# Kernel optimization log

Measured on AMD Instinct MI355X. Metric: run time of the kernel, lower is better.

## Reference

```python
import jax, jax.numpy as jnp
import numpy as np

N, ID, OD, M, S, L = 65536, 16, 8, 1024, 8, 64


def setup_inputs() -> dict:
    key = jax.random.key(0)
    k1, k2, k3, k4, k5, k6 = jax.random.split(key, 6)
    return {
        "x": jax.random.normal(k1, (N, ID), dtype=jnp.float32),
        "inducing_locations": jax.random.uniform(k2, (M, ID), dtype=jnp.float32),
        "inducing_weights": jax.random.normal(k3, (S, OD, M), dtype=jnp.float32),
        "prior_frequency": jax.random.normal(k4, (OD, ID, L), dtype=jnp.float32),
        "prior_phase": jax.random.uniform(k5, (OD, L), dtype=jnp.float32, maxval=2 * np.pi),
        "prior_weights": jax.random.normal(k6, (S, OD, L), dtype=jnp.float32),
    }


def _rbf_matrix(x, z):
    # ExponentiatedQuadratic with amplitude=1, length_scale=1:
    # k(x,z) = exp(-0.5 * ||x - z||^2)
    x2 = jnp.sum(x * x, axis=-1)[:, None]          # [N,1]
    z2 = jnp.sum(z * z, axis=-1)[None, :]          # [1,M]
    sq = jnp.maximum(x2 + z2 - 2.0 * (x @ z.T), 0.0)
    return jnp.exp(-0.5 * sq)                      # [N,M]


def reference(x, inducing_locations, inducing_weights, prior_frequency, prior_phase, prior_weights):
    # ---- prior (random Fourier features) ----
    # spectral_weights for unit RBF: outer_weights = ones((OD,L)), inner_weights = ones((ID,))
    # rescaled_x = x / 1 = x
    # basis_fn_inner_prod: [OD, N, L]
    inner = jnp.einsum('ni,oil->onl', x, prior_frequency)
    basis_fn = jnp.cos(inner + prior_phase[:, None, :])              # [OD,N,L]
    basis_weight = jnp.sqrt(2.0 / prior_frequency.shape[-1]) * prior_weights  # [S,OD,L]
    f_prior = jnp.einsum('onl,sol->son', basis_fn, basis_weight)     # [S,OD,N]

    # ---- data term (kernel matrix + matvec) ----
    K = _rbf_matrix(x, inducing_locations)                           # [N,M]
    f_data = jnp.einsum('nm,som->son', K, inducing_weights)          # [S,OD,N]

    return f_prior + f_data
```

## Files before the change

### kernel.cpp

```cpp
#include <hip/hip_runtime.h>
#include <hip/hip_bf16.h>

#define N_PTS 65536
#define LOG2E 1.4426950408889634f

typedef __attribute__((ext_vector_type(8))) short short8;
typedef __attribute__((ext_vector_type(4))) short short4v;
typedef __attribute__((ext_vector_type(4))) float float4v;

#if __has_builtin(__builtin_amdgcn_exp2f)
#define EXP2F(x) __builtin_amdgcn_exp2f(x)
#else
#define EXP2F(x) exp2f(x)
#endif

__device__ __forceinline__ short f2b(float f) {
    __hip_bfloat16 h = __float2bfloat16(f);
    return *(short*)&h;
}
__device__ __forceinline__ float b2f(short s) {
    __hip_bfloat16 h = *(__hip_bfloat16*)&s;
    return __bfloat162float(h);
}

__global__ __launch_bounds__(256) void prep_kernel(
    const float* __restrict__ z, const float* __restrict__ W,
    const float* __restrict__ F, const float* __restrict__ pw,
    short* __restrict__ zb, short* __restrict__ FbB,
    short* __restrict__ BWd, short* __restrict__ Wtb,
    float* __restrict__ z2h)
{
    int t = blockIdx.x * 256 + threadIdx.x;
    if (t < 16384) {
        zb[t] = f2b(LOG2E * z[t]);
    } else if (t < 17408) {
        int m = t - 16384;
        const float4v* zp = (const float4v*)(z + (size_t)m * 16);
        float s = 0.f;
        #pragma unroll
        for (int k = 0; k < 4; k++) {
            float4v v = zp[k];
            float a0 = b2f(f2b(v.x)), a1 = b2f(f2b(v.y));
            float a2 = b2f(f2b(v.z)), a3 = b2f(f2b(v.w));
            s += a0 * a0 + a1 * a1 + a2 * a2 + a3 * a3;
        }
        z2h[m] = 0.5f * LOG2E * s;
    } else if (t < 25600) {
        int p = t - 17408;
        int o = p >> 10, l = (p >> 4) & 63, i = p & 15;
        FbB[p] = f2b(F[o * 1024 + i * 64 + l]);
    } else if (t < 58368) {
        int p = t - 25600;
        int so = p >> 9, ol = p & 511, o = ol >> 6;
        float v = ((so & 7) == o) ? 0.17677669529663687f * pw[so * 64 + (ol & 63)] : 0.f;
        BWd[p] = f2b(v);
    } else if (t < 123904) {
        int p = t - 58368;
        Wtb[p] = f2b(W[p]);
    }
}

__global__ __launch_bounds__(256, 3) void fused_kernel(
    const float* __restrict__ x, const float* __restrict__ ph,
    const short* __restrict__ zb, const short* __restrict__ FbB,
    const short* __restrict__ BWd, const short* __restrict__ Wtb,
    const float* __restrict__ z2h, float* __restrict__ out)
{
    __shared__ __align__(16) char smem[34816];
    short* tiles = (short*)smem;
    float* phc   = (float*)(smem + 16384);
    float* nz2   = (float*)(smem + 18432);
    float* x2c   = (float*)(smem + 22528);
    float* rbufA = (float*)smem;
    float* rbufB = (float*)(smem + 17408);

    const int tid = threadIdx.x;
    const int lane = tid & 63, w = tid >> 6;
    const int q = lane >> 4, c = lane & 15;
    const int n0 = blockIdx.x * 64;

    for (int i = tid; i < 512; i += 256) phc[i] = ph[i];
    for (int i = tid; i < 1024; i += 256) nz2[i] = -z2h[i];
    if (tid < 64) {
        float s = 0.f;
        const float4v* xr = (const float4v*)(x + (size_t)(n0 + tid) * 16);
        #pragma unroll
        for (int k = 0; k < 4; k++) {
            float4v v = xr[k];
            float a0 = b2f(f2b(v.x)), a1 = b2f(f2b(v.y));
            float a2 = b2f(f2b(v.z)), a3 = b2f(f2b(v.w));
            s += a0 * a0 + a1 * a1 + a2 * a2 + a3 * a3;
        }
        x2c[tid] = 0.5f * LOG2E * s;
    }

    short8 ax[4];
    #pragma unroll
    for (int nt = 0; nt < 4; nt++) {
        ax[nt] = (short8)0;
        if (q < 2) {
            const float4v* xp = (const float4v*)(x + (size_t)(n0 + nt * 16 + c) * 16 + q * 8);
            float4v v0 = xp[0], v1 = xp[1];
            ax[nt][0] = f2b(v0.x); ax[nt][1] = f2b(v0.y);
            ax[nt][2] = f2b(v0.z); ax[nt][3] = f2b(v0.w);
            ax[nt][4] = f2b(v1.x); ax[nt][5] = f2b(v1.y);
            ax[nt][6] = f2b(v1.z); ax[nt][7] = f2b(v1.w);
        }
    }

    float4v acc[4][4];
    #pragma unroll
    for (int a = 0; a < 4; a++)
        #pragma unroll
        for (int nt = 0; nt < 4; nt++) acc[a][nt] = (float4v)(0.f);

    __syncthreads();

    char* myt = (char*)tiles + w * 4096;
    const int swz = (c & 3) << 4;
    const int wb0 = (c * 64 + q * 8) ^ swz;
    const int wb1 = (c * 64 + 32 + q * 8) ^ swz;
    const int rb0 = (c * 64 + q * 16) ^ swz;

    const int mbase = w * 256;
    #pragma unroll 2
    for (int mb = 0; mb < 8; mb++) {
        const int m0 = mbase + mb * 32;
        #pragma unroll
        for (int mh = 0; mh < 2; mh++) {
            short8 bz = (short8)0;
            if (q < 2) bz = *(const short8*)(zb + (size_t)(m0 + mh * 16 + c) * 16 + q * 8);
            float4v c0 = *(const float4v*)(nz2 + m0 + mh * 16 + 4 * q);
            const int wb = mh ? wb1 : wb0;
            #pragma unroll
            for (int nt = 0; nt < 4; nt++) {
                float4v d = __builtin_amdgcn_mfma_f32_16x16x32_bf16(bz, ax[nt], c0, 0, 0, 0);
                short4v pk;
                pk[0] = f2b(EXP2F(d[0])); pk[1] = f2b(EXP2F(d[1]));
                pk[2] = f2b(EXP2F(d[2])); pk[3] = f2b(EXP2F(d[3]));
                *(short4v*)(myt + nt * 1024 + wb) = pk;
            }
        }
        short8 aw[4];
        #pragma unroll
        for (int a = 0; a < 4; a++)
            aw[a] = *(const short8*)(Wtb + (size_t)(a * 16 + c) * 1024 + m0 + q * 8);
        #pragma unroll
        for (int nt = 0; nt < 4; nt++) {
            short8 bb = *(const short8*)(myt + nt * 1024 + rb0);
            #pragma unroll
            for (int a = 0; a < 4; a++)
                acc[a][nt] = __builtin_amdgcn_mfma_f32_16x16x32_bf16(aw[a], bb, acc[a][nt], 0, 0, 0);
        }
    }

    #pragma unroll
    for (int nt = 0; nt < 4; nt++) {
        float sxv = EXP2F(-x2c[nt * 16 + c]);
        #pragma unroll
        for (int a = 0; a < 4; a++) acc[a][nt] *= sxv;
    }

    const int lbase = w * 128;
    #pragma unroll 2
    for (int lb = 0; lb < 4; lb++) {
        const int l0 = lbase + lb * 32;
        #pragma unroll
        for (int mh = 0; mh < 2; mh++) {
            short8 bf = (short8)0;
            if (q < 2) bf = *(const short8*)(FbB + (size_t)(l0 + mh * 16 + c) * 16 + q * 8);
            float4v c0 = *(const float4v*)(phc + l0 + mh * 16 + 4 * q);
            const int wb = mh ? wb1 : wb0;
            #pragma unroll
            for (int nt = 0; nt < 4; nt++) {
                float4v d = __builtin_amdgcn_mfma_f32_16x16x32_bf16(bf, ax[nt], c0, 0, 0, 0);
                short4v pk;
                pk[0] = f2b(__cosf(d[0])); pk[1] = f2b(__cosf(d[1]));
                pk[2] = f2b(__cosf(d[2])); pk[3] = f2b(__cosf(d[3]));
                *(short4v*)(myt + nt * 1024 + wb) = pk;
            }
        }
        short8 aw[4];
        #pragma unroll
        for (int a = 0; a < 4; a++)
            aw[a] = *(const short8*)(BWd + (size_t)(a * 16 + c) * 512 + l0 + q * 8);
        #pragma unroll
        for (int nt = 0; nt < 4; nt++) {
            short8 bb = *(const short8*)(myt + nt * 1024 + rb0);
            #pragma unroll
            for (int a = 0; a < 4; a++)
                acc[a][nt] = __builtin_amdgcn_mfma_f32_16x16x32_bf16(aw[a], bb, acc[a][nt], 0, 0, 0);
        }
    }

    __syncthreads();
    if (w & 1) {
        float* rb = (w == 1) ? rbufA : rbufB;
        #pragma unroll
        for (int a = 0; a < 4; a++)
            #pragma unroll
            for (int nt = 0; nt < 4; nt++)
                #pragma unroll
                for (int r = 0; r < 4; r++)
                    rb[(a * 16 + 4 * q + r) * 68 + nt * 16 + c] = acc[a][nt][r];
    }
    __syncthreads();
    if (!(w & 1)) {
        float* rb = (w == 0) ? rbufA : rbufB;
        #pragma unroll
        for (int a = 0; a < 4; a++)
            #pragma unroll
            for (int nt = 0; nt < 4; nt++)
                #pragma unroll
                for (int r = 0; r < 4; r++) {
                    int idx = (a * 16 + 4 * q + r) * 68 + nt * 16 + c;
                    rb[idx] += acc[a][nt][r];
                }
    }
    __syncthreads();
    #pragma unroll
    for (int k = 0; k < 16; k++) {
        int idx = k * 256 + tid;
        int row = idx >> 6, nn = idx & 63;
        out[(size_t)row * N_PTS + n0 + nn] = rbufA[row * 68 + nn] + rbufB[row * 68 + nn];
    }
}

extern "C" void kernel_launch(void* const* d_in, const int* in_sizes, int n_in,
                              void* d_out, int out_size, void* d_ws, size_t ws_size,
                              hipStream_t stream) {
    const float* x  = (const float*)d_in[0];
    const float* z  = (const float*)d_in[1];
    const float* W  = (const float*)d_in[2];
    const float* F  = (const float*)d_in[3];
    const float* ph = (const float*)d_in[4];
    const float* pw = (const float*)d_in[5];
    float* out = (float*)d_out;

    char* ws = (char*)d_ws;
    short* zb  = (short*)(ws);
    short* FbB = (short*)(ws + 32768);
    short* BWd = (short*)(ws + 49152);
    short* Wtb = (short*)(ws + 114688);
    float* z2h = (float*)(ws + 245760);

    prep_kernel<<<484, 256, 0, stream>>>(z, W, F, pw, zb, FbB, BWd, Wtb, z2h);
    fused_kernel<<<1024, 256, 0, stream>>>(x, ph, zb, FbB, BWd, Wtb, z2h, out);
}
```

Before: 108.6 us.

## Permute inducing rows so MFMA outputs feed the next MFMA directly from registers

Reorders the rows of z, F, phase and the z-norm term in the prep kernel with a permutation chosen so that the accumulator layout of the first MFMA matches the B-operand layout of the second. The exp/cos results then pack straight into short8 register operands, removing the LDS tile store, reload and swizzle. The per-block LDS staging of phase and z-norm is dropped in favour of direct global loads, and launch bounds rise to 4 blocks per CU. The risks are more register pressure from holding the pb arrays and uncached global loads in the inner loop.

After: 110.9 us. 2.1% more time.

```diff
diff --git a/kernel.cpp b/kernel.cpp
--- a/kernel.cpp
+++ b/kernel.cpp
@@ -5,7 +5,6 @@
 #define LOG2E 1.4426950408889634f
 
 typedef __attribute__((ext_vector_type(8))) short short8;
-typedef __attribute__((ext_vector_type(4))) short short4v;
 typedef __attribute__((ext_vector_type(4))) float float4v;
 
 #if __has_builtin(__builtin_amdgcn_exp2f)
@@ -23,19 +22,27 @@
     return __bfloat162float(h);
 }
 
+__device__ __forceinline__ int permrow(int p) {
+    return ((p & 12) << 1) + (p & 3) + ((p >> 4) << 2);
+}
+
 __global__ __launch_bounds__(256) void prep_kernel(
     const float* __restrict__ z, const float* __restrict__ W,
     const float* __restrict__ F, const float* __restrict__ pw,
+    const float* __restrict__ ph,
     short* __restrict__ zb, short* __restrict__ FbB,
     short* __restrict__ BWd, short* __restrict__ Wtb,
-    float* __restrict__ z2h)
+    float* __restrict__ nz2P, float* __restrict__ phP)
 {
     int t = blockIdx.x * 256 + threadIdx.x;
     if (t < 16384) {
-        zb[t] = f2b(LOG2E * z[t]);
+        int row = t >> 4, i = t & 15;
+        int src = (row & ~31) + permrow(row & 31);
+        zb[t] = f2b(LOG2E * z[src * 16 + i]);
     } else if (t < 17408) {
         int m = t - 16384;
-        const float4v* zp = (const float4v*)(z + (size_t)m * 16);
+        int src = (m & ~31) + permrow(m & 31);
+        const float4v* zp = (const float4v*)(z + (size_t)src * 16);
         float s = 0.f;
         #pragma unroll
         for (int k = 0; k < 4; k++) {
@@ -44,10 +51,12 @@
             float a2 = b2f(f2b(v.z)), a3 = b2f(f2b(v.w));
             s += a0 * a0 + a1 * a1 + a2 * a2 + a3 * a3;
         }
-        z2h[m] = 0.5f * LOG2E * s;
+        nz2P[m] = -(0.5f * LOG2E * s);
     } else if (t < 25600) {
         int p = t - 17408;
-        int o = p >> 10, l = (p >> 4) & 63, i = p & 15;
+        int row = p >> 4, i = p & 15;
+        int srow = (row & ~31) + permrow(row & 31);
+        int o = srow >> 6, l = srow & 63;
         FbB[p] = f2b(F[o * 1024 + i * 64 + l]);
     } else if (t < 58368) {
         int p = t - 25600;
@@ -57,30 +66,29 @@
     } else if (t < 123904) {
         int p = t - 58368;
         Wtb[p] = f2b(W[p]);
-    }
-}
-
-__global__ __launch_bounds__(256, 3) void fused_kernel(
-    const float* __restrict__ x, const float* __restrict__ ph,
+    } else {
+        int j = t - 123904;
+        int sj = (j & ~31) + permrow(j & 31);
+        phP[j] = ph[sj];
+    }
+}
+
+__global__ __launch_bounds__(256, 4) void fused_kernel(
+    const float* __restrict__ x,
     const short* __restrict__ zb, const short* __restrict__ FbB,
     const short* __restrict__ BWd, const short* __restrict__ Wtb,
-    const float* __restrict__ z2h, float* __restrict__ out)
+    const float* __restrict__ nz2P, const float* __restrict__ phP,
+    float* __restrict__ out)
 {
-    __shared__ __align__(16) char smem[34816];
-    short* tiles = (short*)smem;
-    float* phc   = (float*)(smem + 16384);
-    float* nz2   = (float*)(smem + 18432);
-    float* x2c   = (float*)(smem + 22528);
-    float* rbufA = (float*)smem;
-    float* rbufB = (float*)(smem + 17408);
+    __shared__ float x2c[64];
+    __shared__ __align__(16) float rbufA[64 * 68];
+    __shared__ __align__(16) float rbufB[64 * 68];
 
     const int tid = threadIdx.x;
     const int lane = tid & 63, w = tid >> 6;
     const int q = lane >> 4, c = lane & 15;
     const int n0 = blockIdx.x * 64;
 
-    for (int i = tid; i < 512; i += 256) phc[i] = ph[i];
-    for (int i = tid; i < 1024; i += 256) nz2[i] = -z2h[i];
     if (tid < 64) {
         float s = 0.f;
         const float4v* xr = (const float4v*)(x + (size_t)(n0 + tid) * 16);
@@ -116,41 +124,35 @@
 
     __syncthreads();
 
-    char* myt = (char*)tiles + w * 4096;
-    const int swz = (c & 3) << 4;
-    const int wb0 = (c * 64 + q * 8) ^ swz;
-    const int wb1 = (c * 64 + 32 + q * 8) ^ swz;
-    const int rb0 = (c * 64 + q * 16) ^ swz;
-
     const int mbase = w * 256;
     #pragma unroll 2
     for (int mb = 0; mb < 8; mb++) {
         const int m0 = mbase + mb * 32;
-        #pragma unroll
-        for (int mh = 0; mh < 2; mh++) {
-            short8 bz = (short8)0;
-            if (q < 2) bz = *(const short8*)(zb + (size_t)(m0 + mh * 16 + c) * 16 + q * 8);
-            float4v c0 = *(const float4v*)(nz2 + m0 + mh * 16 + 4 * q);
-            const int wb = mh ? wb1 : wb0;
-            #pragma unroll
-            for (int nt = 0; nt < 4; nt++) {
-                float4v d = __builtin_amdgcn_mfma_f32_16x16x32_bf16(bz, ax[nt], c0, 0, 0, 0);
-                short4v pk;
-                pk[0] = f2b(EXP2F(d[0])); pk[1] = f2b(EXP2F(d[1]));
-                pk[2] = f2b(EXP2F(d[2])); pk[3] = f2b(EXP2F(d[3]));
-                *(short4v*)(myt + nt * 1024 + wb) = pk;
-            }
-        }
-        short8 aw[4];
-        #pragma unroll
-        for (int a = 0; a < 4; a++)
-            aw[a] = *(const short8*)(Wtb + (size_t)(a * 16 + c) * 1024 + m0 + q * 8);
+        short8 bzA = (short8)0, bzB = (short8)0;
+        if (q < 2) {
+            bzA = *(const short8*)(zb + (size_t)(m0 + c) * 16 + q * 8);
+            bzB = *(const short8*)(zb + (size_t)(m0 + 16 + c) * 16 + q * 8);
+        }
+        float4v c0A = *(const float4v*)(nz2P + m0 + 4 * q);
+        float4v c0B = *(const float4v*)(nz2P + m0 + 16 + 4 * q);
+        short8 pb[4];
         #pragma unroll
         for (int nt = 0; nt < 4; nt++) {
-            short8 bb = *(const short8*)(myt + nt * 1024 + rb0);
-            #pragma unroll
-            for (int a = 0; a < 4; a++)
-                acc[a][nt] = __builtin_amdgcn_mfma_f32_16x16x32_bf16(aw[a], bb, acc[a][nt], 0, 0, 0);
+            float4v dA = __builtin_amdgcn_mfma_f32_16x16x32_bf16(bzA, ax[nt], c0A, 0, 0, 0);
+            float4v dB = __builtin_amdgcn_mfma_f32_16x16x32_bf16(bzB, ax[nt], c0B, 0, 0, 0);
+            short8 t;
+            t[0] = f2b(EXP2F(dA[0])); t[1] = f2b(EXP2F(dA[1]));
+            t[2] = f2b(EXP2F(dA[2])); t[3] = f2b(EXP2F(dA[3]));
+            t[4] = f2b(EXP2F(dB[0])); t[5] = f2b(EXP2F(dB[1]));
+            t[6] = f2b(EXP2F(dB[2])); t[7] = f2b(EXP2F(dB[3]));
+            pb[nt] = t;
+        }
+        #pragma unroll
+        for (int a = 0; a < 4; a++) {
+            short8 aw = *(const short8*)(Wtb + (size_t)(a * 16 + c) * 1024 + m0 + q * 8);
+            #pragma unroll
+            for (int nt = 0; nt < 4; nt++)
+                acc[a][nt] = __builtin_amdgcn_mfma_f32_16x16x32_bf16(aw, pb[nt], acc[a][nt], 0, 0, 0);
         }
     }
 
@@ -165,31 +167,31 @@
     #pragma unroll 2
     for (int lb = 0; lb < 4; lb++) {
         const int l0 = lbase + lb * 32;
-        #pragma unroll
-        for (int mh = 0; mh < 2; mh++) {
-            short8 bf = (short8)0;
-            if (q < 2) bf = *(const short8*)(FbB + (size_t)(l0 + mh * 16 + c) * 16 + q * 8);
-            float4v c0 = *(const float4v*)(phc + l0 + mh * 16 + 4 * q);
-            const int wb = mh ? wb1 : wb0;
-            #pragma unroll
-            for (int nt = 0; nt < 4; nt++) {
-                float4v d = __builtin_amdgcn_mfma_f32_16x16x32_bf16(bf, ax[nt], c0, 0, 0, 0);
-                short4v pk;
-                pk[0] = f2b(__cosf(d[0])); pk[1] = f2b(__cosf(d[1]));
-                pk[2] = f2b(__cosf(d[2])); pk[3] = f2b(__cosf(d[3]));
-                *(short4v*)(myt + nt * 1024 + wb) = pk;
-            }
-        }
-        short8 aw[4];
-        #pragma unroll
-        for (int a = 0; a < 4; a++)
-            aw[a] = *(const short8*)(BWd + (size_t)(a * 16 + c) * 512 + l0 + q * 8);
+        short8 bfA = (short8)0, bfB = (short8)0;
+        if (q < 2) {
+            bfA = *(const short8*)(FbB + (size_t)(l0 + c) * 16 + q * 8);
+            bfB = *(const short8*)(FbB + (size_t)(l0 + 16 + c) * 16 + q * 8);
+        }
+        float4v c0A = *(const float4v*)(phP + l0 + 4 * q);
+        float4v c0B = *(const float4v*)(phP + l0 + 16 + 4 * q);
+        short8 pb[4];
         #pragma unroll
         for (int nt = 0; nt < 4; nt++) {
-            short8 bb = *(const short8*)(myt + nt * 1024 + rb0);
-            #pragma unroll
-            for (int a = 0; a < 4; a++)
-                acc[a][nt] = __builtin_amdgcn_mfma_f32_16x16x32_bf16(aw[a], bb, acc[a][nt], 0, 0, 0);
+            float4v dA = __builtin_amdgcn_mfma_f32_16x16x32_bf16(bfA, ax[nt], c0A, 0, 0, 0);
+            float4v dB = __builtin_amdgcn_mfma_f32_16x16x32_bf16(bfB, ax[nt], c0B, 0, 0, 0);
+            short8 t;
+            t[0] = f2b(__cosf(dA[0])); t[1] = f2b(__cosf(dA[1]));
+            t[2] = f2b(__cosf(dA[2])); t[3] = f2b(__cosf(dA[3]));
+            t[4] = f2b(__cosf(dB[0])); t[5] = f2b(__cosf(dB[1]));
+            t[6] = f2b(__cosf(dB[2])); t[7] = f2b(__cosf(dB[3]));
+            pb[nt] = t;
+        }
+        #pragma unroll
+        for (int a = 0; a < 4; a++) {
+            short8 aw = *(const short8*)(BWd + (size_t)(a * 16 + c) * 512 + l0 + q * 8);
+            #pragma unroll
+            for (int nt = 0; nt < 4; nt++)
+                acc[a][nt] = __builtin_amdgcn_mfma_f32_16x16x32_bf16(aw, pb[nt], acc[a][nt], 0, 0, 0);
         }
     }
 
@@ -238,12 +240,13 @@
     float* out = (float*)d_out;
 
     char* ws = (char*)d_ws;
-    short* zb  = (short*)(ws);
-    short* FbB = (short*)(ws + 32768);
-    short* BWd = (short*)(ws + 49152);
-    short* Wtb = (short*)(ws + 114688);
-    float* z2h = (float*)(ws + 245760);
-
-    prep_kernel<<<484, 256, 0, stream>>>(z, W, F, pw, zb, FbB, BWd, Wtb, z2h);
-    fused_kernel<<<1024, 256, 0, stream>>>(x, ph, zb, FbB, BWd, Wtb, z2h, out);
-}
+    short* zb   = (short*)(ws);
+    short* FbB  = (short*)(ws + 32768);
+    short* BWd  = (short*)(ws + 49152);
+    short* Wtb  = (short*)(ws + 114688);
+    float* nz2P = (float*)(ws + 245760);
+    float* phP  = (float*)(ws + 249856);
+
+    prep_kernel<<<486, 256, 0, stream>>>(z, W, F, pw, ph, zb, FbB, BWd, Wtb, nz2P, phP);
+    fused_kernel<<<1024, 256, 0, stream>>>(x, zb, FbB, BWd, Wtb, nz2P, phP, out);
+}
```
